# Optimization experiments

Measured on AMD Instinct MI355X. Metric: run time of the kernel, lower is better.

The kernel has to match this reference:

```python
import jax, jax.numpy as jnp
import numpy as np

B, N, K = 8, 8192, 8192   # batch, out_features, in_features
PACK = 8
# maybe_pack_idxs places original column offset POS[b] into nibble b
POS = [0, 2, 4, 6, 1, 3, 5, 7]
# inverse permutation: original offset p comes from nibble INV[p]
INV = jnp.array([0, 4, 1, 5, 2, 6, 3, 7], dtype=jnp.int32)


def setup_inputs() -> dict:
    key = jax.random.key(0)
    k1, k2 = jax.random.split(key)
    x = jax.random.normal(k1, (B, K), dtype=jnp.float32)
    # random 4-bit codebook indices, then pack exactly like maybe_pack_idxs
    idxs = jax.random.randint(k2, (N, K), 0, 16, dtype=jnp.int32)
    g = idxs.reshape(N, K // PACK, PACK)
    packed = jnp.zeros((N, K // PACK), dtype=jnp.int32)
    for b, p in enumerate(POS):
        packed = packed + (g[..., p] << jnp.int32(4 * b))
    return {"input": x, "Qidxs": packed}


def decompress_weight(Qidxs):
    # Qidxs: [N, K/8] int32 -> W: [N, K] float32
    shifts = (jnp.arange(PACK, dtype=jnp.int32) * 4)
    nibbles = (Qidxs[..., None] >> shifts) & 0xF       # [N, K/8, 8], nibble order
    unpacked = nibbles[..., INV]                        # restore original column order
    # grid = arange(-8, 8) + 0.5  =>  value = idx - 7.5
    return unpacked.reshape(N, K).astype(jnp.float32) - 7.5


def reference(input, Qidxs):
    W = decompress_weight(Qidxs)          # [N, K]
    return input @ W.T                    # [B, N]
```

## Files before the change

kernel.cpp:

```cpp
#include <hip/hip_runtime.h>
#include <hip/hip_fp16.h>
#include <stdint.h>


typedef _Float16 half8 __attribute__((ext_vector_type(8)));
typedef float floatx4 __attribute__((ext_vector_type(4)));

union H2U { unsigned u; __half2 h; };
union V4H8 { uint4 u4; half8 h8; };

__device__ __forceinline__ unsigned unpack_even(unsigned w, __half2 c1, __half2 c2) {
    H2U t; t.u = (w & 0x000F000Fu) | 0x64006400u;
    t.h = __hadd2(__hadd2(t.h, c1), c2);
    return t.u;
}
__device__ __forceinline__ unsigned unpack_odd(unsigned w, __half2 cs, __half2 cc) {
    H2U t; t.u = (w & 0x00F000F0u) | 0x64006400u;
    t.h = __hfma2(t.h, cs, cc);
    return t.u;
}

__device__ __forceinline__ void gload_lds16(const void* g, void* l) {
    __builtin_amdgcn_global_load_lds(
        (const __attribute__((address_space(1))) unsigned*)g,
        (__attribute__((address_space(3))) unsigned*)l, 16, 0, 0);
}

#define TPITCH 528
#define NWV    8
#define BWAVE  8192
#define REDOFF (NWV * BWAVE)
#define LDS_BYTES (REDOFF + NWV * 128 * 4)

__global__ void build_atable(const float* __restrict__ x, char* __restrict__ tbl)
{
    const int S = blockIdx.x;
    const int t = threadIdx.x;
    if (t > 32) return;
    uint4 v = make_uint4(0u, 0u, 0u, 0u);
    if (t < 32) {
        const int u = t >> 3, r = t & 7;
        const float4* x4 = (const float4*)x;
        float4 fa = x4[r * 2048 + 8 * S + 2 * u];
        float4 fb = x4[r * 2048 + 8 * S + 2 * u + 1];
        H2U a0, a1, a2, a3;
        a0.h = __floats2half2_rn(fa.x, fa.y);
        a1.h = __floats2half2_rn(fa.z, fa.w);
        a2.h = __floats2half2_rn(fb.x, fb.y);
        a3.h = __floats2half2_rn(fb.z, fb.w);
        v = make_uint4(a0.u, a1.u, a2.u, a3.u);
    }
    const int slot = (t < 32) ? t : 32;
    *(uint4*)(tbl + S * TPITCH + slot * 16) = v;
}

__global__ __launch_bounds__(512, 4)
void hi4b_gemm(const char* __restrict__ atbl, const int* __restrict__ q,
               float* __restrict__ out)
{
    extern __shared__ char lds[];
    const int tid  = threadIdx.x;
    const int lane = tid & 63;
    const int wv   = tid >> 6;
    const int n0   = blockIdx.x * 16;

    const int r16 = lane & 15;
    const int u4  = lane >> 4;

    {
        const int uu = lane >> 5, cc = lane & 31;
        const char* gq = (const char*)q;
        char* ldst = lds + wv * BWAVE;
        #pragma unroll
        for (int j = 0; j < 8; ++j) {
            const int row = 2 * j + uu;
            const char* src = gq + (size_t)(n0 + row) * 4096 + wv * 512
                            + ((cc ^ (row & 7)) << 4);
            gload_lds16(src, ldst + j * 1024);
        }
    }
    __builtin_amdgcn_sched_barrier(0);

    const int  slot = (r16 < 8) ? (u4 * 8 + r16) : 32;
    const char* ap  = atbl + (wv * 32) * TPITCH + slot * 16;

    uint4 T0[4], T1[4];
    auto refill = [&](uint4 (&T)[4], int t) {
        const char* p = ap + t * (4 * TPITCH);
        #pragma unroll
        for (int i = 0; i < 4; ++i)
            T[i] = *(const uint4*)(p + i * TPITCH);
    };
    refill(T0, 0);
    refill(T1, 1);

    asm volatile("s_waitcnt vmcnt(0)" ::: "memory");
    __builtin_amdgcn_sched_barrier(0);

    const __half2 c1 = __floats2half2_rn(-1024.0f, -1024.0f);
    const __half2 c2 = __floats2half2_rn(-7.5f, -7.5f);
    const __half2 cs = __floats2half2_rn(0.0625f, 0.0625f);
    const __half2 cc = __floats2half2_rn(-71.5f, -71.5f);

    floatx4 acc = {0.0f, 0.0f, 0.0f, 0.0f};
    const char* bp = lds + wv * BWAVE + r16 * 512 + u4 * 4;
    const int sx = (r16 & 7) << 4;

    auto comp4 = [&](uint4 (&T)[4], int t) {
        #pragma unroll
        for (int i = 0; i < 4; ++i) {
            const int s = 4 * t + i;
            unsigned w  = *(const unsigned*)(bp + (((s << 4)) ^ sx));
            unsigned w8 = w >> 8;
            V4H8 Bf;
            Bf.u4.x = unpack_even(w,  c1, c2);
            Bf.u4.y = unpack_odd (w,  cs, cc);
            Bf.u4.z = unpack_even(w8, c1, c2);
            Bf.u4.w = unpack_odd (w8, cs, cc);
            V4H8 A;  A.u4 = T[i];
            acc = __builtin_amdgcn_mfma_f32_16x16x32_f16(A.h8, Bf.h8, acc, 0, 0, 0);
        }
    };

    comp4(T0, 0); refill(T0, 2);
    comp4(T1, 1); refill(T1, 3);
    comp4(T0, 2); refill(T0, 4);
    comp4(T1, 3); refill(T1, 5);
    comp4(T0, 4); refill(T0, 6);
    comp4(T1, 5); refill(T1, 7);
    comp4(T0, 6);
    comp4(T1, 7);

    {
        float* red = (float*)(lds + REDOFF) + wv * 128;
        if (u4 < 2) {
            #pragma unroll
            for (int r = 0; r < 4; ++r)
                red[(u4 * 4 + r) * 16 + r16] = acc[r];
        }
    }
    __syncthreads();
    if (tid < 128) {
        const float* rd = (const float*)(lds + REDOFF);
        float sm = 0.0f;
        #pragma unroll
        for (int w = 0; w < NWV; ++w)
            sm += rd[w * 128 + tid];
        out[(tid >> 4) * 8192 + n0 + (tid & 15)] = sm;
    }
}

extern "C" void kernel_launch(void* const* d_in, const int* in_sizes, int n_in,
                              void* d_out, int out_size, void* d_ws, size_t ws_size,
                              hipStream_t stream)
{
    const float* x = (const float*)d_in[0];
    const int*   q = (const int*)d_in[1];
    float* out = (float*)d_out;
    char*  tbl = (char*)d_ws;

    hipLaunchKernelGGL(build_atable, dim3(256), dim3(64), 0, stream, x, tbl);
    hipLaunchKernelGGL(hi4b_gemm, dim3(512), dim3(512), LDS_BYTES, stream,
                       tbl, q, out);
}
```

Before: 17.42 us.

## Fuse fp32-to-fp16 activation conversion into GEMM and drop the pre-pass kernel

Removes the separate build_atable kernel that converted x to an fp16 table in workspace. The GEMM now loads fp32 x directly, converts it to half2 in registers, and masks the unused rows to zero. Loads and conversions are double-buffered against the MFMA loop using an explicit vmcnt wait. This saves one kernel launch and a workspace round trip, but each block converts x redundantly, doubles the activation bytes loaded, and adds register pressure.

```diff
diff --git a/kernel.cpp b/kernel.cpp
--- a/kernel.cpp
+++ b/kernel.cpp
@@ -26,36 +26,13 @@
         (__attribute__((address_space(3))) unsigned*)l, 16, 0, 0);
 }
 
-#define TPITCH 528
 #define NWV    8
 #define BWAVE  8192
 #define REDOFF (NWV * BWAVE)
 #define LDS_BYTES (REDOFF + NWV * 128 * 4)
 
-__global__ void build_atable(const float* __restrict__ x, char* __restrict__ tbl)
-{
-    const int S = blockIdx.x;
-    const int t = threadIdx.x;
-    if (t > 32) return;
-    uint4 v = make_uint4(0u, 0u, 0u, 0u);
-    if (t < 32) {
-        const int u = t >> 3, r = t & 7;
-        const float4* x4 = (const float4*)x;
-        float4 fa = x4[r * 2048 + 8 * S + 2 * u];
-        float4 fb = x4[r * 2048 + 8 * S + 2 * u + 1];
-        H2U a0, a1, a2, a3;
-        a0.h = __floats2half2_rn(fa.x, fa.y);
-        a1.h = __floats2half2_rn(fa.z, fa.w);
-        a2.h = __floats2half2_rn(fb.x, fb.y);
-        a3.h = __floats2half2_rn(fb.z, fb.w);
-        v = make_uint4(a0.u, a1.u, a2.u, a3.u);
-    }
-    const int slot = (t < 32) ? t : 32;
-    *(uint4*)(tbl + S * TPITCH + slot * 16) = v;
-}
-
 __global__ __launch_bounds__(512, 4)
-void hi4b_gemm(const char* __restrict__ atbl, const int* __restrict__ q,
+void hi4b_gemm(const float* __restrict__ x, const int* __restrict__ q,
                float* __restrict__ out)
 {
     extern __shared__ char lds[];
@@ -81,21 +58,31 @@
     }
     __builtin_amdgcn_sched_barrier(0);
 
-    const int  slot = (r16 < 8) ? (u4 * 8 + r16) : 32;
-    const char* ap  = atbl + (wv * 32) * TPITCH + slot * 16;
+    const float4* xr4 = (const float4*)x + (size_t)(r16 & 7) * 2048
+                      + wv * 256 + 2 * u4;
+    const unsigned rowmask = (r16 < 8) ? 0xFFFFFFFFu : 0u;
 
-    uint4 T0[4], T1[4];
-    auto refill = [&](uint4 (&T)[4], int t) {
-        const char* p = ap + t * (4 * TPITCH);
+    float4 LA[8], LB[8];
+    auto loadF = [&](float4 (&L)[8], int t) {
         #pragma unroll
-        for (int i = 0; i < 4; ++i)
-            T[i] = *(const uint4*)(p + i * TPITCH);
+        for (int i = 0; i < 4; ++i) {
+            L[2 * i]     = xr4[32 * t + 8 * i];
+            L[2 * i + 1] = xr4[32 * t + 8 * i + 1];
+        }
     };
-    refill(T0, 0);
-    refill(T1, 1);
-
-    asm volatile("s_waitcnt vmcnt(0)" ::: "memory");
-    __builtin_amdgcn_sched_barrier(0);
+    uint4 F[4];
+    auto cvtF = [&](float4 (&L)[8]) {
+        #pragma unroll
+        for (int i = 0; i < 4; ++i) {
+            H2U a0, a1, a2, a3;
+            a0.h = __floats2half2_rn(L[2*i].x,   L[2*i].y);
+            a1.h = __floats2half2_rn(L[2*i].z,   L[2*i].w);
+            a2.h = __floats2half2_rn(L[2*i+1].x, L[2*i+1].y);
+            a3.h = __floats2half2_rn(L[2*i+1].z, L[2*i+1].w);
+            F[i] = make_uint4(a0.u & rowmask, a1.u & rowmask,
+                              a2.u & rowmask, a3.u & rowmask);
+        }
+    };
 
     const __half2 c1 = __floats2half2_rn(-1024.0f, -1024.0f);
     const __half2 c2 = __floats2half2_rn(-7.5f, -7.5f);
@@ -106,30 +93,34 @@
     const char* bp = lds + wv * BWAVE + r16 * 512 + u4 * 4;
     const int sx = (r16 & 7) << 4;
 
-    auto comp4 = [&](uint4 (&T)[4], int t) {
+    auto comp4 = [&](int t) {
         #pragma unroll
         for (int i = 0; i < 4; ++i) {
             const int s = 4 * t + i;
-            unsigned w  = *(const unsigned*)(bp + (((s << 4)) ^ sx));
+            unsigned w  = *(const unsigned*)(bp + ((s << 4) ^ sx));
             unsigned w8 = w >> 8;
             V4H8 Bf;
             Bf.u4.x = unpack_even(w,  c1, c2);
             Bf.u4.y = unpack_odd (w,  cs, cc);
             Bf.u4.z = unpack_even(w8, c1, c2);
             Bf.u4.w = unpack_odd (w8, cs, cc);
-            V4H8 A;  A.u4 = T[i];
+            V4H8 A;  A.u4 = F[i];
             acc = __builtin_amdgcn_mfma_f32_16x16x32_f16(A.h8, Bf.h8, acc, 0, 0, 0);
         }
     };
 
-    comp4(T0, 0); refill(T0, 2);
-    comp4(T1, 1); refill(T1, 3);
-    comp4(T0, 2); refill(T0, 4);
-    comp4(T1, 3); refill(T1, 5);
-    comp4(T0, 4); refill(T0, 6);
-    comp4(T1, 5); refill(T1, 7);
-    comp4(T0, 6);
-    comp4(T1, 7);
+    loadF(LA, 0); loadF(LB, 1);
+    cvtF(LA);
+    asm volatile("s_waitcnt vmcnt(8)" ::: "memory");
+    __builtin_amdgcn_sched_barrier(0);
+    comp4(0); loadF(LA, 2);
+    cvtF(LB); comp4(1); loadF(LB, 3);
+    cvtF(LA); comp4(2); loadF(LA, 4);
+    cvtF(LB); comp4(3); loadF(LB, 5);
+    cvtF(LA); comp4(4); loadF(LA, 6);
+    cvtF(LB); comp4(5); loadF(LB, 7);
+    cvtF(LA); comp4(6);
+    cvtF(LB); comp4(7);
 
     {
         float* red = (float*)(lds + REDOFF) + wv * 128;
@@ -144,8 +135,8 @@
         const float* rd = (const float*)(lds + REDOFF);
         float sm = 0.0f;
         #pragma unroll
-        for (int w = 0; w < NWV; ++w)
-            sm += rd[w * 128 + tid];
+        for (int wi = 0; wi < NWV; ++wi)
+            sm += rd[wi * 128 + tid];
         out[(tid >> 4) * 8192 + n0 + (tid & 15)] = sm;
     }
 }
@@ -157,9 +148,7 @@
     const float* x = (const float*)d_in[0];
     const int*   q = (const int*)d_in[1];
     float* out = (float*)d_out;
-    char*  tbl = (char*)d_ws;
 
-    hipLaunchKernelGGL(build_atable, dim3(256), dim3(64), 0, stream, x, tbl);
     hipLaunchKernelGGL(hi4b_gemm, dim3(512), dim3(512), LDS_BYTES, stream,
-                       tbl, q, out);
+                       x, q, out);
 }
```

New measurement: 36.67 us. 2.1x slower.
